# Kernel optimization log

Hardware: AMD Instinct MI355X
Metric: run time of the kernel (lower is better)

Reference implementation:

```python
import jax, jax.numpy as jnp
import numpy as np

NUM_FORMULAS = 1024
INPUT_DIM = 256
BATCH = 2048


def setup_inputs() -> dict:
    key = jax.random.key(0)
    k_x, k_mu, k_sigma = jax.random.split(key, 3)
    inputs = jax.random.normal(k_x, (BATCH, INPUT_DIM), dtype=jnp.float32)
    # keras random_normal initializer default stddev = 0.05
    mu = 0.05 * jax.random.normal(k_mu, (NUM_FORMULAS, INPUT_DIM), dtype=jnp.float32)
    sigma = 0.05 * jax.random.normal(k_sigma, (1, NUM_FORMULAS, INPUT_DIM), dtype=jnp.float32)
    temperature = jnp.float32(2.0)
    return {"inputs": inputs, "mu": mu, "sigma": sigma, "temperature": temperature}


def reference(inputs, mu, sigma, temperature):
    # diff: (batch, num_formulas, dim)
    diff = inputs[:, None, :] - mu[None, :, :]
    # weighted L2 norm over feature dim -> (batch, num_formulas)
    dist = jnp.sqrt(jnp.sum(jnp.square(diff * sigma), axis=-1))
    loc = jnp.exp(-dist)
    # sigmoid-gated temperature, softmax over formulas (last axis)
    return jax.nn.softmax(jax.nn.sigmoid(temperature) * loc, axis=-1)
```

## Files before the change

### kernel.cpp

```cpp
#include <hip/hip_runtime.h>
#include <math.h>

#define NF 1024
#define DIM 256
#define BATCH 2048
#define K 512
#define BMF 16
#define NCC 4
#define CF (NF / NCC)
#define KS 32
#define NSTEP (K / KS)

#define WS_C_OFF  (NF * K * 2)
#define WS_RP_OFF (WS_C_OFF + NF * 4)

typedef __attribute__((ext_vector_type(8))) short short8;
typedef __attribute__((ext_vector_type(4))) float f32x4;

__device__ __forceinline__ unsigned short f2bf(float f) {
    unsigned u = __float_as_uint(f);
    u += 0x7fffu + ((u >> 16) & 1u);
    return (unsigned short)(u >> 16);
}

__device__ __forceinline__ void gl_lds16(const ushort* g, ushort* l) {
    __builtin_amdgcn_global_load_lds(
        (const __attribute__((address_space(1))) void*)g,
        (__attribute__((address_space(3))) void*)l, 16, 0, 0);
}

__global__ __launch_bounds__(256) void k_prep(const float* __restrict__ mu,
                                              const float* __restrict__ sigma,
                                              uint4* __restrict__ Bb4,
                                              float* __restrict__ c) {
    const int t = threadIdx.x;
    const int f = blockIdx.x * 4 + (t >> 6);
    const int sq = t & 63;
    const float4 mv = *(const float4*)&mu[f * DIM + sq * 4];
    const float4 sv = *(const float4*)&sigma[f * DIM + sq * 4];

    uint4 pk; float cp = 0.f;
    {
        const float s2x = sv.x * sv.x;
        pk.x = (unsigned)f2bf(s2x) | ((unsigned)f2bf(-2.0f * s2x * mv.x) << 16);
        cp += s2x * mv.x * mv.x;
        const float s2y = sv.y * sv.y;
        pk.y = (unsigned)f2bf(s2y) | ((unsigned)f2bf(-2.0f * s2y * mv.y) << 16);
        cp += s2y * mv.y * mv.y;
        const float s2z = sv.z * sv.z;
        pk.z = (unsigned)f2bf(s2z) | ((unsigned)f2bf(-2.0f * s2z * mv.z) << 16);
        cp += s2z * mv.z * mv.z;
        const float s2w = sv.w * sv.w;
        pk.w = (unsigned)f2bf(s2w) | ((unsigned)f2bf(-2.0f * s2w * mv.w) << 16);
        cp += s2w * mv.w * mv.w;
    }
    Bb4[(f >> 8) * 16384 + (sq >> 2) * 1024 + (sq & 3) * 256 + (f & 255)] = pk;

    #pragma unroll
    for (int off = 32; off > 0; off >>= 1) cp += __shfl_down(cp, off, 64);
    if ((t & 63) == 0) c[f] = cp;
}

__global__ __launch_bounds__(256, 3) void k_main(const float* __restrict__ x,
                                                 const ushort* __restrict__ Bb,
                                                 const float* __restrict__ c,
                                                 const float* __restrict__ temp,
                                                 float* __restrict__ out,
                                                 float* __restrict__ rowPartial) {
    const int t = threadIdx.x;
    const int w = t >> 6;
    const int lane = t & 63;
    const int m16 = lane & 15;
    const int q = lane >> 4;
    const int r0 = blockIdx.x * BMF;
    const int cc = blockIdx.y;

    __shared__ __align__(16) ushort ldsA[BMF * K];
    __shared__ __align__(16) ushort ldsB[2][CF * KS];
    __shared__ float wsum[4][BMF];

    #pragma unroll
    for (int h = 0; h < 4; ++h) {
        const int u = h * 256 + t;
        const int row = u >> 6, kc = u & 63;
        const float4 v = *(const float4*)&x[(r0 + row) * DIM + kc * 4];
        uint4 pk;
        pk.x = (unsigned)f2bf(v.x * v.x) | ((unsigned)f2bf(v.x) << 16);
        pk.y = (unsigned)f2bf(v.y * v.y) | ((unsigned)f2bf(v.y) << 16);
        pk.z = (unsigned)f2bf(v.z * v.z) | ((unsigned)f2bf(v.z) << 16);
        pk.w = (unsigned)f2bf(v.w * v.w) | ((unsigned)f2bf(v.w) << 16);
        *(uint4*)&ldsA[(row * 64 + (kc ^ (row & 7))) * 8] = pk;
    }

    f32x4 acc[4];
    #pragma unroll
    for (int ct = 0; ct < 4; ++ct) acc[ct] = (f32x4){0.f, 0.f, 0.f, 0.f};

    const ushort* bsrc = Bb + cc * (CF * K);

    #pragma unroll
    for (int i = 0; i < 4; ++i) {
        const int u = i * 256 + t;
        gl_lds16(bsrc + u * 8, &ldsB[0][u * 8]);
    }

    #pragma unroll 1
    for (int s = 0; s < NSTEP; ++s) {
        __syncthreads();
        if (s + 1 < NSTEP) {
            const ushort* src = bsrc + (s + 1) * (CF * KS);
            ushort* dst = &ldsB[(s + 1) & 1][0];
            #pragma unroll
            for (int i = 0; i < 4; ++i) {
                const int u = i * 256 + t;
                gl_lds16(src + u * 8, dst + u * 8);
            }
        }
        const ushort* bcur = &ldsB[s & 1][0];
        const int kcq = s * 4 + q;
        const short8 av = *(const short8*)&ldsA[(m16 * 64 + (kcq ^ (m16 & 7))) * 8];
        #pragma unroll
        for (int ct = 0; ct < 4; ++ct) {
            const int fl = w * 64 + ct * 16 + m16;
            const short8 bv = *(const short8*)&bcur[q * (CF * 8) + fl * 8];
            acc[ct] = __builtin_amdgcn_mfma_f32_16x16x32_bf16(av, bv, acc[ct], 0, 0, 0);
        }
    }

    const float g = 1.0f / (1.0f + __expf(-temp[0]));
    float s4[4] = {0.f, 0.f, 0.f, 0.f};
    #pragma unroll
    for (int ct = 0; ct < 4; ++ct) {
        const int fcol = cc * CF + w * 64 + ct * 16 + m16;
        const float cn = c[fcol];
        #pragma unroll
        for (int i = 0; i < 4; ++i) {
            const float dist2 = acc[ct][i] + cn;
            const float dist = sqrtf(fmaxf(dist2, 0.0f));
            const float p = __expf(g * __expf(-dist));
            out[(r0 + q * 4 + i) * NF + fcol] = p;
            s4[i] += p;
        }
    }
    #pragma unroll
    for (int i = 0; i < 4; ++i) {
        #pragma unroll
        for (int mask = 1; mask < 16; mask <<= 1)
            s4[i] += __shfl_xor(s4[i], mask, 64);
    }
    if (m16 == 0) {
        #pragma unroll
        for (int i = 0; i < 4; ++i) wsum[w][q * 4 + i] = s4[i];
    }
    __syncthreads();
    if (t < BMF)
        rowPartial[cc * BATCH + r0 + t] =
            (wsum[0][t] + wsum[1][t]) + (wsum[2][t] + wsum[3][t]);
}

__global__ __launch_bounds__(256) void k_norm(float* __restrict__ out,
                                              const float* __restrict__ rowPartial) {
    const int row = blockIdx.x;
    const float ssum = (rowPartial[row] + rowPartial[BATCH + row]) +
                       (rowPartial[2 * BATCH + row] + rowPartial[3 * BATCH + row]);
    const float inv = 1.0f / ssum;
    float4* o4 = (float4*)(out + row * NF);
    float4 v = o4[threadIdx.x];
    v.x *= inv; v.y *= inv; v.z *= inv; v.w *= inv;
    o4[threadIdx.x] = v;
}

extern "C" void kernel_launch(void* const* d_in, const int* in_sizes, int n_in,
                              void* d_out, int out_size, void* d_ws, size_t ws_size,
                              hipStream_t stream) {
    const float* x     = (const float*)d_in[0];
    const float* mu    = (const float*)d_in[1];
    const float* sigma = (const float*)d_in[2];
    const float* temp  = (const float*)d_in[3];
    float* out = (float*)d_out;

    char* ws = (char*)d_ws;
    ushort* Bb         = (ushort*)ws;
    float*  c          = (float*)(ws + WS_C_OFF);
    float*  rowPartial = (float*)(ws + WS_RP_OFF);

    k_prep<<<NF / 4, 256, 0, stream>>>(mu, sigma, (uint4*)Bb, c);

    dim3 g2(BATCH / BMF, NCC);
    k_main<<<g2, 256, 0, stream>>>(x, Bb, c, temp, out, rowPartial);

    k_norm<<<BATCH, 256, 0, stream>>>(out, rowPartial);
}
```

Before: 82.70 us.

## Fuse prep, main and normalize into one cooperative kernel with grid syncs

Replaces the three launches (prep, main GEMM-softmax, normalize) with a single cooperative kernel of 512 blocks that uses grid-wide syncs between phases. Probabilities stay in registers across the second grid sync and are written to the output once, already normalized, instead of being written and then re-read and rewritten by a separate normalize kernel. This removes two launch gaps and a full read-modify-write pass over the output, at the cost of two grid barriers and a requirement that all 512 blocks be co-resident. If the cooperative launch fails, it falls back to the old three-kernel path.

Result: slower. 171.0 us (+106.7%).

```diff
diff --git a/kernel.cpp b/kernel.cpp
--- a/kernel.cpp
+++ b/kernel.cpp
@@ -1,5 +1,8 @@
 #include <hip/hip_runtime.h>
+#include <hip/hip_cooperative_groups.h>
 #include <math.h>
+
+namespace cg = cooperative_groups;
 
 #define NF 1024
 #define DIM 256
@@ -29,6 +32,153 @@
         (__attribute__((address_space(3))) void*)l, 16, 0, 0);
 }
 
+__global__ __launch_bounds__(256, 2) void k_all(const float* __restrict__ x,
+                                                const float* __restrict__ mu,
+                                                const float* __restrict__ sigma,
+                                                const float* __restrict__ temp,
+                                                float* __restrict__ out,
+                                                ushort* __restrict__ Bb,
+                                                float* __restrict__ c,
+                                                float* __restrict__ rowPartial) {
+    const int t = threadIdx.x;
+    const int w = t >> 6;
+    const int lane = t & 63;
+    const int m16 = lane & 15;
+    const int q = lane >> 4;
+    const int bid = blockIdx.x;
+    const int rg = bid & 127, cc = bid >> 7;
+    const int r0 = rg * BMF;
+
+    __shared__ __align__(16) ushort ldsA[BMF * K];
+    __shared__ __align__(16) ushort ldsB[2][CF * KS];
+    __shared__ float wsum[4][BMF];
+    __shared__ float rowInv[BMF];
+
+    if (w < 2) {
+        const int f = bid * 2 + w;
+        const float4 mv = *(const float4*)&mu[f * DIM + lane * 4];
+        const float4 sv = *(const float4*)&sigma[f * DIM + lane * 4];
+        uint4 pk; float cp = 0.f;
+        {
+            const float s2x = sv.x * sv.x;
+            pk.x = (unsigned)f2bf(s2x) | ((unsigned)f2bf(-2.0f * s2x * mv.x) << 16);
+            cp += s2x * mv.x * mv.x;
+            const float s2y = sv.y * sv.y;
+            pk.y = (unsigned)f2bf(s2y) | ((unsigned)f2bf(-2.0f * s2y * mv.y) << 16);
+            cp += s2y * mv.y * mv.y;
+            const float s2z = sv.z * sv.z;
+            pk.z = (unsigned)f2bf(s2z) | ((unsigned)f2bf(-2.0f * s2z * mv.z) << 16);
+            cp += s2z * mv.z * mv.z;
+            const float s2w = sv.w * sv.w;
+            pk.w = (unsigned)f2bf(s2w) | ((unsigned)f2bf(-2.0f * s2w * mv.w) << 16);
+            cp += s2w * mv.w * mv.w;
+        }
+        ((uint4*)Bb)[(f >> 8) * 16384 + (lane >> 2) * 1024 + (lane & 3) * 256 + (f & 255)] = pk;
+        #pragma unroll
+        for (int off = 32; off > 0; off >>= 1) cp += __shfl_down(cp, off, 64);
+        if (lane == 0) c[f] = cp;
+    }
+
+    #pragma unroll
+    for (int h = 0; h < 4; ++h) {
+        const int u = h * 256 + t;
+        const int row = u >> 6, kc = u & 63;
+        const float4 v = *(const float4*)&x[(r0 + row) * DIM + kc * 4];
+        uint4 pk;
+        pk.x = (unsigned)f2bf(v.x * v.x) | ((unsigned)f2bf(v.x) << 16);
+        pk.y = (unsigned)f2bf(v.y * v.y) | ((unsigned)f2bf(v.y) << 16);
+        pk.z = (unsigned)f2bf(v.z * v.z) | ((unsigned)f2bf(v.z) << 16);
+        pk.w = (unsigned)f2bf(v.w * v.w) | ((unsigned)f2bf(v.w) << 16);
+        *(uint4*)&ldsA[(row * 64 + (kc ^ (row & 7))) * 8] = pk;
+    }
+
+    cg::this_grid().sync();
+
+    f32x4 acc[4];
+    #pragma unroll
+    for (int ct = 0; ct < 4; ++ct) acc[ct] = (f32x4){0.f, 0.f, 0.f, 0.f};
+
+    const ushort* bsrc = Bb + cc * (CF * K);
+
+    #pragma unroll
+    for (int i = 0; i < 4; ++i) {
+        const int u = i * 256 + t;
+        gl_lds16(bsrc + u * 8, &ldsB[0][u * 8]);
+    }
+
+    #pragma unroll 1
+    for (int s = 0; s < NSTEP; ++s) {
+        __syncthreads();
+        if (s + 1 < NSTEP) {
+            const ushort* src = bsrc + (s + 1) * (CF * KS);
+            ushort* dst = &ldsB[(s + 1) & 1][0];
+            #pragma unroll
+            for (int i = 0; i < 4; ++i) {
+                const int u = i * 256 + t;
+                gl_lds16(src + u * 8, dst + u * 8);
+            }
+        }
+        const ushort* bcur = &ldsB[s & 1][0];
+        const int kcq = s * 4 + q;
+        const short8 av = *(const short8*)&ldsA[(m16 * 64 + (kcq ^ (m16 & 7))) * 8];
+        #pragma unroll
+        for (int ct = 0; ct < 4; ++ct) {
+            const int fl = w * 64 + ct * 16 + m16;
+            const short8 bv = *(const short8*)&bcur[q * (CF * 8) + fl * 8];
+            acc[ct] = __builtin_amdgcn_mfma_f32_16x16x32_bf16(av, bv, acc[ct], 0, 0, 0);
+        }
+    }
+
+    const float g = 1.0f / (1.0f + __expf(-temp[0]));
+    float s4[4] = {0.f, 0.f, 0.f, 0.f};
+    #pragma unroll
+    for (int ct = 0; ct < 4; ++ct) {
+        const float cn = c[cc * CF + w * 64 + ct * 16 + m16];
+        #pragma unroll
+        for (int i = 0; i < 4; ++i) {
+            const float dist2 = acc[ct][i] + cn;
+            const float dist = sqrtf(fmaxf(dist2, 0.0f));
+            const float p = __expf(g * __expf(-dist));
+            acc[ct][i] = p;
+            s4[i] += p;
+        }
+    }
+    #pragma unroll
+    for (int i = 0; i < 4; ++i) {
+        #pragma unroll
+        for (int mask = 1; mask < 16; mask <<= 1)
+            s4[i] += __shfl_xor(s4[i], mask, 64);
+    }
+    if (m16 == 0) {
+        #pragma unroll
+        for (int i = 0; i < 4; ++i) wsum[w][q * 4 + i] = s4[i];
+    }
+    __syncthreads();
+    if (t < BMF)
+        rowPartial[cc * BATCH + r0 + t] =
+            (wsum[0][t] + wsum[1][t]) + (wsum[2][t] + wsum[3][t]);
+
+    cg::this_grid().sync();
+
+    if (t < BMF) {
+        const int row = r0 + t;
+        const float ssum = (rowPartial[row] + rowPartial[BATCH + row]) +
+                           (rowPartial[2 * BATCH + row] + rowPartial[3 * BATCH + row]);
+        rowInv[t] = 1.0f / ssum;
+    }
+    __syncthreads();
+    float inv[4];
+    #pragma unroll
+    for (int i = 0; i < 4; ++i) inv[i] = rowInv[q * 4 + i];
+    #pragma unroll
+    for (int ct = 0; ct < 4; ++ct) {
+        const int fcol = cc * CF + w * 64 + ct * 16 + m16;
+        #pragma unroll
+        for (int i = 0; i < 4; ++i)
+            out[(r0 + q * 4 + i) * NF + fcol] = acc[ct][i] * inv[i];
+    }
+}
+
 __global__ __launch_bounds__(256) void k_prep(const float* __restrict__ mu,
                                               const float* __restrict__ sigma,
                                               uint4* __restrict__ Bb4,
@@ -38,7 +188,6 @@
     const int sq = t & 63;
     const float4 mv = *(const float4*)&mu[f * DIM + sq * 4];
     const float4 sv = *(const float4*)&sigma[f * DIM + sq * 4];
-
     uint4 pk; float cp = 0.f;
     {
         const float s2x = sv.x * sv.x;
@@ -55,7 +204,6 @@
         cp += s2w * mv.w * mv.w;
     }
     Bb4[(f >> 8) * 16384 + (sq >> 2) * 1024 + (sq & 3) * 256 + (f & 255)] = pk;
-
     #pragma unroll
     for (int off = 32; off > 0; off >>= 1) cp += __shfl_down(cp, off, 64);
     if ((t & 63) == 0) c[f] = cp;
@@ -97,7 +245,6 @@
     for (int ct = 0; ct < 4; ++ct) acc[ct] = (f32x4){0.f, 0.f, 0.f, 0.f};
 
     const ushort* bsrc = Bb + cc * (CF * K);
-
     #pragma unroll
     for (int i = 0; i < 4; ++i) {
         const int u = i * 256 + t;
@@ -184,10 +331,14 @@
     float*  c          = (float*)(ws + WS_C_OFF);
     float*  rowPartial = (float*)(ws + WS_RP_OFF);
 
-    k_prep<<<NF / 4, 256, 0, stream>>>(mu, sigma, (uint4*)Bb, c);
-
-    dim3 g2(BATCH / BMF, NCC);
-    k_main<<<g2, 256, 0, stream>>>(x, Bb, c, temp, out, rowPartial);
-
-    k_norm<<<BATCH, 256, 0, stream>>>(out, rowPartial);
-}
+    void* args[] = {(void*)&x, (void*)&mu, (void*)&sigma, (void*)&temp,
+                    (void*)&out, (void*)&Bb, (void*)&c, (void*)&rowPartial};
+    hipError_t err = hipLaunchCooperativeKernel((const void*)k_all, dim3(512),
+                                                dim3(256), args, 0, stream);
+    if (err != hipSuccess) {
+        k_prep<<<NF / 4, 256, 0, stream>>>(mu, sigma, (uint4*)Bb, c);
+        dim3 g2(BATCH / BMF, NCC);
+        k_main<<<g2, 256, 0, stream>>>(x, Bb, c, temp, out, rowPartial);
+        k_norm<<<BATCH, 256, 0, stream>>>(out, rowPartial);
+    }
+}
```

## Load B operands directly from global into registers with double buffering

Applied to the files above, without the earlier changes.

Replaces the LDS double-buffered staging of the B matrix (via global_load_lds plus a barrier every step) with direct per-lane global loads into register double buffers, unrolling the K loop by two. This removes the per-step __syncthreads and LDS traffic for B, but each wave now fetches its own B slices from global/L2 with no sharing across waves. The occupancy hint is lowered from 3 to 2 blocks per SIMD to make room for the extra registers.

Result: faster. 77.70 us (-6.0%).

```diff
diff --git a/kernel.cpp b/kernel.cpp
--- a/kernel.cpp
+++ b/kernel.cpp
@@ -21,12 +21,6 @@
     unsigned u = __float_as_uint(f);
     u += 0x7fffu + ((u >> 16) & 1u);
     return (unsigned short)(u >> 16);
-}
-
-__device__ __forceinline__ void gl_lds16(const ushort* g, ushort* l) {
-    __builtin_amdgcn_global_load_lds(
-        (const __attribute__((address_space(1))) void*)g,
-        (__attribute__((address_space(3))) void*)l, 16, 0, 0);
 }
 
 __global__ __launch_bounds__(256) void k_prep(const float* __restrict__ mu,
@@ -61,7 +55,7 @@
     if ((t & 63) == 0) c[f] = cp;
 }
 
-__global__ __launch_bounds__(256, 3) void k_main(const float* __restrict__ x,
+__global__ __launch_bounds__(256, 2) void k_main(const float* __restrict__ x,
                                                  const ushort* __restrict__ Bb,
                                                  const float* __restrict__ c,
                                                  const float* __restrict__ temp,
@@ -76,7 +70,6 @@
     const int cc = blockIdx.y;
 
     __shared__ __align__(16) ushort ldsA[BMF * K];
-    __shared__ __align__(16) ushort ldsB[2][CF * KS];
     __shared__ float wsum[4][BMF];
 
     #pragma unroll
@@ -96,34 +89,38 @@
     #pragma unroll
     for (int ct = 0; ct < 4; ++ct) acc[ct] = (f32x4){0.f, 0.f, 0.f, 0.f};
 
-    const ushort* bsrc = Bb + cc * (CF * K);
+    const ushort* bp = Bb + cc * (CF * K) + q * (CF * 8) + (w * 64 + m16) * 8;
 
+    short8 bA[4], bB[4];
     #pragma unroll
-    for (int i = 0; i < 4; ++i) {
-        const int u = i * 256 + t;
-        gl_lds16(bsrc + u * 8, &ldsB[0][u * 8]);
-    }
+    for (int ct = 0; ct < 4; ++ct)
+        bA[ct] = *(const short8*)(bp + ct * 128);
+
+    __syncthreads();
 
     #pragma unroll 1
-    for (int s = 0; s < NSTEP; ++s) {
-        __syncthreads();
-        if (s + 1 < NSTEP) {
-            const ushort* src = bsrc + (s + 1) * (CF * KS);
-            ushort* dst = &ldsB[(s + 1) & 1][0];
+    for (int s = 0; s < NSTEP; s += 2) {
+        #pragma unroll
+        for (int ct = 0; ct < 4; ++ct)
+            bB[ct] = *(const short8*)(bp + (s + 1) * 8192 + ct * 128);
+        {
+            const int kcq = s * 4 + q;
+            const short8 av = *(const short8*)&ldsA[(m16 * 64 + (kcq ^ (m16 & 7))) * 8];
             #pragma unroll
-            for (int i = 0; i < 4; ++i) {
-                const int u = i * 256 + t;
-                gl_lds16(src + u * 8, dst + u * 8);
-            }
+            for (int ct = 0; ct < 4; ++ct)
+                acc[ct] = __builtin_amdgcn_mfma_f32_16x16x32_bf16(av, bA[ct], acc[ct], 0, 0, 0);
         }
-        const ushort* bcur = &ldsB[s & 1][0];
-        const int kcq = s * 4 + q;
-        const short8 av = *(const short8*)&ldsA[(m16 * 64 + (kcq ^ (m16 & 7))) * 8];
-        #pragma unroll
-        for (int ct = 0; ct < 4; ++ct) {
-            const int fl = w * 64 + ct * 16 + m16;
-            const short8 bv = *(const short8*)&bcur[q * (CF * 8) + fl * 8];
-            acc[ct] = __builtin_amdgcn_mfma_f32_16x16x32_bf16(av, bv, acc[ct], 0, 0, 0);
+        if (s + 2 < NSTEP) {
+            #pragma unroll
+            for (int ct = 0; ct < 4; ++ct)
+                bA[ct] = *(const short8*)(bp + (s + 2) * 8192 + ct * 128);
+        }
+        {
+            const int kcq = (s + 1) * 4 + q;
+            const short8 av = *(const short8*)&ldsA[(m16 * 64 + (kcq ^ (m16 & 7))) * 8];
+            #pragma unroll
+            for (int ct = 0; ct < 4; ++ct)
+                acc[ct] = __builtin_amdgcn_mfma_f32_16x16x32_bf16(av, bB[ct], acc[ct], 0, 0, 0);
         }
     }
 
```
